# Kernel tuning notes

Hardware: AMD Instinct MI355X
Metric: run time of the kernel (lower is better)

The kernel has to match this reference:

```python
import jax, jax.numpy as jnp
import numpy as np

HIDDEN = 4096
N_HEADS = 32
N_KV_HEADS = 8
HEAD_DIM = 128
MAX_POS = 4096
N_GROUPS = N_HEADS // N_KV_HEADS  # 4


def _sincos_table():
    # create_sinusoidal_positions(MAX_POS, HEAD_DIM) -> [MAX_POS, 1, 2*HEAD_DIM]
    inv_freq = 1.0 / 10000 ** (np.arange(0, HEAD_DIM, 2) / HEAD_DIM)
    freqs = np.einsum('i,j->ij', np.arange(MAX_POS), inv_freq).astype('float32')
    emb = np.concatenate((freqs, freqs), axis=-1)  # [MAX_POS, HEAD_DIM]
    out = np.concatenate((np.sin(emb)[:, None, :], np.cos(emb)[:, None, :]), axis=-1)
    return jnp.asarray(out[:, :, :MAX_POS])  # slice is a no-op since 2*HEAD_DIM < MAX_POS

_SINCOS = _sincos_table()


def _rotate_half(t):
    half = t.shape[-1] // 2
    return jnp.concatenate((-t[..., half:], t[..., :half]), axis=-1)


def setup_inputs() -> dict:
    key = jax.random.key(0)
    ks = jax.random.split(key, 9)
    B, S = 1, 2048
    scale = 0.02
    return {
        'hidden_states': jax.random.normal(ks[0], (B, S, HIDDEN), jnp.float32),
        'attention_mask': jnp.ones((B, 1, 1, S), jnp.bool_),
        'position_ids': jnp.broadcast_to(jnp.arange(S, dtype=jnp.int32)[None, :], (B, S)),
        'Wq': jax.random.normal(ks[1], (HIDDEN, N_HEADS * HEAD_DIM), jnp.float32) * scale,
        'bq': jnp.zeros((N_HEADS * HEAD_DIM,), jnp.float32),
        'Wk': jax.random.normal(ks[2], (HIDDEN, N_KV_HEADS * HEAD_DIM), jnp.float32) * scale,
        'bk': jnp.zeros((N_KV_HEADS * HEAD_DIM,), jnp.float32),
        'Wv': jax.random.normal(ks[3], (HIDDEN, N_KV_HEADS * HEAD_DIM), jnp.float32) * scale,
        'bv': jnp.zeros((N_KV_HEADS * HEAD_DIM,), jnp.float32),
        'Wo': jax.random.normal(ks[4], (N_HEADS * HEAD_DIM, HIDDEN), jnp.float32) * scale,
        'bo': jnp.zeros((HIDDEN,), jnp.float32),
    }


def reference(hidden_states, attention_mask, position_ids, Wq, bq, Wk, bk, Wv, bv, Wo, bo):
    B, S, _ = hidden_states.shape
    # QKV projections + split heads
    q = (hidden_states @ Wq + bq).reshape(B, S, N_HEADS, HEAD_DIM)
    k = (hidden_states @ Wk + bk).reshape(B, S, N_KV_HEADS, HEAD_DIM)
    v = (hidden_states @ Wv + bv).reshape(B, S, N_KV_HEADS, HEAD_DIM)
    # Rotary embedding: sincos[position_ids] -> [B,S,1,2*HEAD_DIM]
    sincos = _SINCOS[position_ids]
    sin_pos, cos_pos = jnp.split(sincos, 2, axis=-1)  # each [B,S,1,HEAD_DIM]
    k = k * cos_pos + _rotate_half(k) * sin_pos
    q = q * cos_pos + _rotate_half(q) * sin_pos
    # Causal mask combined with padding mask
    causal = jnp.tril(jnp.ones((S, S), jnp.bool_))[None, None]  # [1,1,S,S]
    mask = jnp.logical_and(attention_mask, causal)  # [B,1,S,S]
    # GQA: repeat kv heads
    k = jnp.repeat(k, N_GROUPS, axis=2)  # [B,S,H,D]
    v = jnp.repeat(v, N_GROUPS, axis=2)
    bias = jnp.where(mask, 0.0, jnp.finfo(jnp.float32).min).astype(jnp.float32)
    scores = jnp.einsum('bqhd,bkhd->bhqk', q, k) / jnp.sqrt(jnp.float32(HEAD_DIM)) + bias
    attn_weights = jax.nn.softmax(scores, axis=-1)  # [B,H,S,S]
    attn_output = jnp.einsum('bhqk,bkhd->bqhd', attn_weights, v).reshape(B, S, N_HEADS * HEAD_DIM)
    return attn_output @ Wo + bo
```

## Files before the change

kernel.cpp:

```cpp
#include <hip/hip_runtime.h>
#include <hip/hip_bf16.h>
#include <math.h>

typedef __bf16 bf16x8 __attribute__((ext_vector_type(8)));
typedef __bf16 bf16x4 __attribute__((ext_vector_type(4)));
typedef float  f32x4  __attribute__((ext_vector_type(4)));
typedef unsigned int u32;

#define S_LEN 2048
#define HID   4096
#define NH    32
#define NKV   8
#define HD    128

__device__ inline void gld_lds16(const __bf16* g, __bf16* l) {
  __builtin_amdgcn_global_load_lds((const __attribute__((address_space(1))) u32*)g,
                                   (__attribute__((address_space(3))) u32*)l,
                                   16, 0, 0);
}

__global__ void cast_bf16(const float* __restrict__ in, __bf16* __restrict__ out, int n4) {
  int i = blockIdx.x * blockDim.x + threadIdx.x;
  if (i < n4) {
    float4 v = ((const float4*)in)[i];
    bf16x4 o;
    o[0] = (__bf16)v.x; o[1] = (__bf16)v.y; o[2] = (__bf16)v.z; o[3] = (__bf16)v.w;
    ((bf16x4*)out)[i] = o;
  }
}

template <typename T>
__global__ void transpose_cast(const T* __restrict__ in, __bf16* __restrict__ out,
                               int ldi, int ldo) {
  __shared__ float tile[32][33];
  const int c0 = blockIdx.x * 32, r0 = blockIdx.y * 32;
  const int tx = threadIdx.x, ty = threadIdx.y;
  for (int j = 0; j < 32; j += 8)
    tile[ty + j][tx] = (float)in[(size_t)(r0 + ty + j) * ldi + c0 + tx];
  __syncthreads();
  for (int j = 0; j < 32; j += 8)
    out[(size_t)(c0 + ty + j) * ldo + r0 + tx] = (__bf16)tile[tx][ty + j];
}

__global__ void concat_bias(const float* __restrict__ bk, const float* __restrict__ bv,
                            float* __restrict__ out) {
  int i = blockIdx.x * blockDim.x + threadIdx.x;
  if (i < 2048) out[i] = (i < 1024) ? bk[i] : bv[i - 1024];
}

template <typename CT>
__global__ __launch_bounds__(256) void gemm_bt(const __bf16* __restrict__ A,
                                               const __bf16* __restrict__ Bt,
                                               const float* __restrict__ bias,
                                               CT* __restrict__ C,
                                               int M, int N, int K) {
  __shared__ __bf16 As[128 * 32];
  __shared__ __bf16 Bs[128 * 32];
  const int tid  = threadIdx.x;
  const int lane = tid & 63;
  const int lrow = lane & 15, quad = lane >> 4;
  const int wave = tid >> 6;
  const int wm = (wave & 1) * 64, wn = (wave >> 1) * 64;
  const int m0 = blockIdx.y * 128, n0 = blockIdx.x * 128;

  f32x4 acc[4][4] = {};

  const int c1 = tid, c2 = tid + 256;
  const __bf16* a1 = A + (size_t)(m0 + (c1 >> 2)) * K + (c1 & 3) * 8;
  const __bf16* a2 = A + (size_t)(m0 + (c2 >> 2)) * K + (c2 & 3) * 8;
  const __bf16* b1 = Bt + (size_t)(n0 + (c1 >> 2)) * K + (c1 & 3) * 8;
  const __bf16* b2 = Bt + (size_t)(n0 + (c2 >> 2)) * K + (c2 & 3) * 8;
  __bf16* As1 = As + c1 * 8; __bf16* As2 = As + c2 * 8;
  __bf16* Bs1 = Bs + c1 * 8; __bf16* Bs2 = Bs + c2 * 8;

  for (int k0 = 0; k0 < K; k0 += 32) {
    __syncthreads();
    gld_lds16(a1 + k0, As1);
    gld_lds16(a2 + k0, As2);
    gld_lds16(b1 + k0, Bs1);
    gld_lds16(b2 + k0, Bs2);
    __syncthreads();

    bf16x8 af[4], bfr[4];
#pragma unroll
    for (int t = 0; t < 4; t++) {
      af[t]  = *(const bf16x8*)(As + (wm + t * 16 + lrow) * 32 + quad * 8);
      bfr[t] = *(const bf16x8*)(Bs + (wn + t * 16 + lrow) * 32 + quad * 8);
    }
#pragma unroll
    for (int i = 0; i < 4; i++)
#pragma unroll
      for (int j = 0; j < 4; j++)
        acc[i][j] = __builtin_amdgcn_mfma_f32_16x16x32_bf16(af[i], bfr[j], acc[i][j], 0, 0, 0);
  }

#pragma unroll
  for (int i = 0; i < 4; i++) {
    const int row = m0 + wm + i * 16 + quad * 4;
#pragma unroll
    for (int j = 0; j < 4; j++) {
      const int col = n0 + wn + j * 16 + lrow;
      const float b = bias[col];
#pragma unroll
      for (int r = 0; r < 4; r++)
        C[(size_t)(row + r) * N + col] = (CT)(acc[i][j][r] + b);
    }
  }
}

__global__ void rope_inplace(__bf16* __restrict__ Q, __bf16* __restrict__ KV,
                             const int* __restrict__ pos_ids) {
  const int s = blockIdx.y;
  const int t = blockIdx.x * blockDim.x + threadIdx.x;
  const int h = t >> 6, j = t & 63;
  const float pos = (float)pos_ids[s];
  const float inv_freq = __builtin_exp2f((float)j * -0.2076205059304601f);
  const float ang = pos * inv_freq;
  float sn, cs;
  sincosf(ang, &sn, &cs);
  if (h < NH) {
    __bf16* p = Q + (size_t)s * HID + h * HD + j;
    const float x0 = (float)p[0], x1 = (float)p[64];
    p[0]  = (__bf16)(x0 * cs - x1 * sn);
    p[64] = (__bf16)(x1 * cs + x0 * sn);
  } else {
    const int hk = h - NH;
    __bf16* p = KV + (size_t)s * 2048 + hk * HD + j;
    const float x0 = (float)p[0], x1 = (float)p[64];
    p[0]  = (__bf16)(x0 * cs - x1 * sn);
    p[64] = (__bf16)(x1 * cs + x0 * sn);
  }
}

__global__ __launch_bounds__(256) void flash_attn(const __bf16* __restrict__ Qb,
                                                  const __bf16* __restrict__ Kb,
                                                  const __bf16* __restrict__ Vt,
                                                  __bf16* __restrict__ attn, int ldk) {
  __shared__ __bf16 Ks[2][32 * 128];
  __shared__ __bf16 Vs[2][128 * 32];
  __shared__ __bf16 Plds[4][2][16][40];
  const int tid  = threadIdx.x;
  const int wave = tid >> 6;
  const int lane = tid & 63;
  const int lrow = lane & 15, quad = lane >> 4;

  const int c = blockIdx.x & 255, p = blockIdx.x >> 8;
  const int h = c >> 3;
  const int xh = c & 7;
  const int xx = p ? xh : 15 - xh;
  const int bq0 = xx * 128;
  const int kvh = h >> 2;
  const int T0 = bq0 + wave * 16;
  const int T1 = T0 + 64;
  const int kend = bq0 + 128;

  const int cK1 = tid, cK2 = tid + 256;
  const int cV1 = tid, cV2 = tid + 256;
  const __bf16* kg1 = Kb + (size_t)(cK1 & 31) * ldk + kvh * HD + (cK1 >> 5) * 8;
  const __bf16* kg2 = Kb + (size_t)(cK2 & 31) * ldk + kvh * HD + (cK2 >> 5) * 8;
  const __bf16* vg1 = Vt + (size_t)(kvh * HD + (cV1 & 127)) * S_LEN + (cV1 >> 7) * 8;
  const __bf16* vg2 = Vt + (size_t)(kvh * HD + (cV2 & 127)) * S_LEN + (cV2 >> 7) * 8;

  bf16x8 qf[2][4];
#pragma unroll
  for (int m = 0; m < 2; m++) {
    const __bf16* qbase = Qb + (size_t)(T0 + m * 64 + lrow) * HID + h * HD + quad * 8;
#pragma unroll
    for (int kc = 0; kc < 4; kc++) qf[m][kc] = *(const bf16x8*)(qbase + kc * 32);
  }

  f32x4 o[2][8] = {};
  f32x4 lac[2] = {};
  bf16x8 ones;
#pragma unroll
  for (int j = 0; j < 8; j++) ones[j] = (__bf16)1.0f;

  const float cs = 0.08838834764831845f * 1.44269504088896f;

  gld_lds16(kg1, &Ks[0][cK1 * 8]);
  gld_lds16(kg2, &Ks[0][cK2 * 8]);
  gld_lds16(vg1, &Vs[0][cV1 * 8]);
  gld_lds16(vg2, &Vs[0][cV2 * 8]);

  int cur = 0;
  for (int kb = 0; kb < kend; kb += 32) {
    __syncthreads();
    if (kb + 32 < kend) {
      const int nxt = cur ^ 1;
      gld_lds16(kg1 + (size_t)(kb + 32) * ldk, &Ks[nxt][cK1 * 8]);
      gld_lds16(kg2 + (size_t)(kb + 32) * ldk, &Ks[nxt][cK2 * 8]);
      gld_lds16(vg1 + (kb + 32), &Vs[nxt][cV1 * 8]);
      gld_lds16(vg2 + (kb + 32), &Vs[nxt][cV2 * 8]);
    }

    bf16x8 kf0[4], kf1[4];
#pragma unroll
    for (int kc = 0; kc < 4; kc++) {
      kf0[kc] = *(const bf16x8*)(&Ks[cur][((kc * 4 + quad) * 32 + lrow) * 8]);
      kf1[kc] = *(const bf16x8*)(&Ks[cur][((kc * 4 + quad) * 32 + 16 + lrow) * 8]);
    }
    f32x4 s[2][2] = {};
#pragma unroll
    for (int kc = 0; kc < 4; kc++) {
      s[0][0] = __builtin_amdgcn_mfma_f32_16x16x32_bf16(qf[0][kc], kf0[kc], s[0][0], 0, 0, 0);
      s[0][1] = __builtin_amdgcn_mfma_f32_16x16x32_bf16(qf[0][kc], kf1[kc], s[0][1], 0, 0, 0);
      s[1][0] = __builtin_amdgcn_mfma_f32_16x16x32_bf16(qf[1][kc], kf0[kc], s[1][0], 0, 0, 0);
      s[1][1] = __builtin_amdgcn_mfma_f32_16x16x32_bf16(qf[1][kc], kf1[kc], s[1][1], 0, 0, 0);
    }
#pragma unroll
    for (int m = 0; m < 2; m++) {
      const int Tm = m ? T1 : T0;
#pragma unroll
      for (int n = 0; n < 2; n++) {
        const int col = kb + n * 16 + lrow;
#pragma unroll
        for (int r = 0; r < 4; r++) {
          const int row = Tm + quad * 4 + r;
          const float pv = (col <= row) ? __builtin_exp2f(s[m][n][r] * cs) : 0.0f;
          Plds[wave][m][quad * 4 + r][n * 16 + lrow] = (__bf16)pv;
        }
      }
    }
    bf16x8 pf0 = *(const bf16x8*)(&Plds[wave][0][lrow][quad * 8]);
    bf16x8 pf1 = *(const bf16x8*)(&Plds[wave][1][lrow][quad * 8]);
#pragma unroll
    for (int dt = 0; dt < 8; dt++) {
      bf16x8 vf = *(const bf16x8*)(&Vs[cur][(quad * 128 + dt * 16 + lrow) * 8]);
      o[0][dt] = __builtin_amdgcn_mfma_f32_16x16x32_bf16(pf0, vf, o[0][dt], 0, 0, 0);
      o[1][dt] = __builtin_amdgcn_mfma_f32_16x16x32_bf16(pf1, vf, o[1][dt], 0, 0, 0);
    }
    lac[0] = __builtin_amdgcn_mfma_f32_16x16x32_bf16(pf0, ones, lac[0], 0, 0, 0);
    lac[1] = __builtin_amdgcn_mfma_f32_16x16x32_bf16(pf1, ones, lac[1], 0, 0, 0);
    cur ^= 1;
  }

#pragma unroll
  for (int m = 0; m < 2; m++) {
    const int Tm = m ? T1 : T0;
#pragma unroll
    for (int r = 0; r < 4; r++) {
      const float inv_l = 1.0f / lac[m][r];
      const size_t rowoff = (size_t)(Tm + quad * 4 + r) * HID + h * HD;
#pragma unroll
      for (int dt = 0; dt < 8; dt++)
        attn[rowoff + dt * 16 + lrow] = (__bf16)(o[m][dt][r] * inv_l);
    }
  }
}

extern "C" void kernel_launch(void* const* d_in, const int* in_sizes, int n_in,
                              void* d_out, int out_size, void* d_ws, size_t ws_size,
                              hipStream_t stream) {
  const float* hs = (const float*)d_in[0];
  const int* pos = (const int*)d_in[2];
  const float* Wq = (const float*)d_in[3];
  const float* bq = (const float*)d_in[4];
  const float* Wk = (const float*)d_in[5];
  const float* bk = (const float*)d_in[6];
  const float* Wv = (const float*)d_in[7];
  const float* bv = (const float*)d_in[8];
  const float* Wo = (const float*)d_in[9];
  const float* bo = (const float*)d_in[10];
  float* out = (float*)d_out;
  char* ws = (char*)d_ws;
  char* oc = (char*)d_out;

  __bf16* bHS   = (__bf16*)(ws + 0);
  __bf16* bWT   = (__bf16*)(ws + ((size_t)16 << 20));
  __bf16* bAttn = bHS;
  __bf16* bQ   = (__bf16*)(oc + 0);
  __bf16* bKV  = (__bf16*)(oc + ((size_t)16 << 20));
  __bf16* bVt  = (__bf16*)(oc + ((size_t)24 << 20));
  float*  bKVb = (float*)(oc + ((size_t)28 << 20));

  dim3 tb(32, 8);

  cast_bf16<<<8192, 256, 0, stream>>>(hs, bHS, (S_LEN * HID) / 4);
  transpose_cast<float><<<dim3(128, 128), tb, 0, stream>>>(Wq, bWT, 4096, 4096);
  gemm_bt<__bf16><<<dim3(32, 16), 256, 0, stream>>>(bHS, bWT, bq, bQ, 2048, 4096, 4096);
  transpose_cast<float><<<dim3(32, 128), tb, 0, stream>>>(Wk, bWT, 1024, 4096);
  transpose_cast<float><<<dim3(32, 128), tb, 0, stream>>>(Wv, bWT + (size_t)1024 * 4096, 1024, 4096);
  concat_bias<<<8, 256, 0, stream>>>(bk, bv, bKVb);
  gemm_bt<__bf16><<<dim3(16, 16), 256, 0, stream>>>(bHS, bWT, bKVb, bKV, 2048, 2048, 4096);
  rope_inplace<<<dim3(10, 2048), 256, 0, stream>>>(bQ, bKV, pos);
  transpose_cast<__bf16><<<dim3(32, 64), tb, 0, stream>>>(bKV + 1024, bVt, 2048, 2048);
  flash_attn<<<512, 256, 0, stream>>>(bQ, bKV, bVt, bAttn, 2048);
  transpose_cast<float><<<dim3(128, 128), tb, 0, stream>>>(Wo, bWT, 4096, 4096);
  gemm_bt<float><<<dim3(32, 16), 256, 0, stream>>>(bAttn, bWT, bo, out, 2048, 4096, 4096);
}
```

Before: 637.4 us.

## Deepen GEMM K tile and use rotated LDS layouts for GEMM and attention loads

The GEMM now stages a 64-wide K slice per iteration with four 16-byte loads per thread. The LDS tiles are row-major with a per-row rotation of the 8-element chunks, which is meant to avoid bank conflicts on MFMA fragment reads. The attention kernel switches its K and V LDS staging to the same rotated row-major scheme, with fragment offsets precomputed once per thread. This halves the number of barrier pairs in the GEMM and coalesces global reads, at the cost of doubled GEMM LDS and extra offset registers.

```diff
diff --git a/kernel.cpp b/kernel.cpp
--- a/kernel.cpp
+++ b/kernel.cpp
@@ -54,8 +54,8 @@
                                                const float* __restrict__ bias,
                                                CT* __restrict__ C,
                                                int M, int N, int K) {
-  __shared__ __bf16 As[128 * 32];
-  __shared__ __bf16 Bs[128 * 32];
+  __shared__ __bf16 As[128 * 64];
+  __shared__ __bf16 Bs[128 * 64];
   const int tid  = threadIdx.x;
   const int lane = tid & 63;
   const int lrow = lane & 15, quad = lane >> 4;
@@ -65,33 +65,55 @@
 
   f32x4 acc[4][4] = {};
 
-  const int c1 = tid, c2 = tid + 256;
-  const __bf16* a1 = A + (size_t)(m0 + (c1 >> 2)) * K + (c1 & 3) * 8;
-  const __bf16* a2 = A + (size_t)(m0 + (c2 >> 2)) * K + (c2 & 3) * 8;
-  const __bf16* b1 = Bt + (size_t)(n0 + (c1 >> 2)) * K + (c1 & 3) * 8;
-  const __bf16* b2 = Bt + (size_t)(n0 + (c2 >> 2)) * K + (c2 & 3) * 8;
-  __bf16* As1 = As + c1 * 8; __bf16* As2 = As + c2 * 8;
-  __bf16* Bs1 = Bs + c1 * 8; __bf16* Bs2 = Bs + c2 * 8;
-
-  for (int k0 = 0; k0 < K; k0 += 32) {
+  const __bf16* aP[4];
+  const __bf16* bP[4];
+  __bf16* aL[4];
+  __bf16* bL[4];
+#pragma unroll
+  for (int s = 0; s < 4; s++) {
+    const int c = tid + 256 * s;
+    const int row = c >> 3;
+    const int kc = ((c & 7) + row) & 7;
+    aP[s] = A + (size_t)(m0 + row) * K + kc * 8;
+    bP[s] = Bt + (size_t)(n0 + row) * K + kc * 8;
+    aL[s] = As + c * 8;
+    bL[s] = Bs + c * 8;
+  }
+
+  int offA[2][4], offB[2][4];
+#pragma unroll
+  for (int h = 0; h < 2; h++)
+#pragma unroll
+    for (int t = 0; t < 4; t++) {
+      const int ra = wm + t * 16 + lrow;
+      const int rb = wn + t * 16 + lrow;
+      offA[h][t] = (ra * 8 + ((h * 4 + quad - ra) & 7)) * 8;
+      offB[h][t] = (rb * 8 + ((h * 4 + quad - rb) & 7)) * 8;
+    }
+
+  for (int k0 = 0; k0 < K; k0 += 64) {
     __syncthreads();
-    gld_lds16(a1 + k0, As1);
-    gld_lds16(a2 + k0, As2);
-    gld_lds16(b1 + k0, Bs1);
-    gld_lds16(b2 + k0, Bs2);
+#pragma unroll
+    for (int s = 0; s < 4; s++) {
+      gld_lds16(aP[s] + k0, aL[s]);
+      gld_lds16(bP[s] + k0, bL[s]);
+    }
     __syncthreads();
 
-    bf16x8 af[4], bfr[4];
-#pragma unroll
-    for (int t = 0; t < 4; t++) {
-      af[t]  = *(const bf16x8*)(As + (wm + t * 16 + lrow) * 32 + quad * 8);
-      bfr[t] = *(const bf16x8*)(Bs + (wn + t * 16 + lrow) * 32 + quad * 8);
-    }
-#pragma unroll
-    for (int i = 0; i < 4; i++)
-#pragma unroll
-      for (int j = 0; j < 4; j++)
-        acc[i][j] = __builtin_amdgcn_mfma_f32_16x16x32_bf16(af[i], bfr[j], acc[i][j], 0, 0, 0);
+#pragma unroll
+    for (int h = 0; h < 2; h++) {
+      bf16x8 af[4], bfr[4];
+#pragma unroll
+      for (int t = 0; t < 4; t++) {
+        af[t]  = *(const bf16x8*)(As + offA[h][t]);
+        bfr[t] = *(const bf16x8*)(Bs + offB[h][t]);
+      }
+#pragma unroll
+      for (int i = 0; i < 4; i++)
+#pragma unroll
+        for (int j = 0; j < 4; j++)
+          acc[i][j] = __builtin_amdgcn_mfma_f32_16x16x32_bf16(af[i], bfr[j], acc[i][j], 0, 0, 0);
+    }
   }
 
 #pragma unroll
@@ -154,12 +176,34 @@
   const int T1 = T0 + 64;
   const int kend = bq0 + 128;
 
-  const int cK1 = tid, cK2 = tid + 256;
-  const int cV1 = tid, cV2 = tid + 256;
-  const __bf16* kg1 = Kb + (size_t)(cK1 & 31) * ldk + kvh * HD + (cK1 >> 5) * 8;
-  const __bf16* kg2 = Kb + (size_t)(cK2 & 31) * ldk + kvh * HD + (cK2 >> 5) * 8;
-  const __bf16* vg1 = Vt + (size_t)(kvh * HD + (cV1 & 127)) * S_LEN + (cV1 >> 7) * 8;
-  const __bf16* vg2 = Vt + (size_t)(kvh * HD + (cV2 & 127)) * S_LEN + (cV2 >> 7) * 8;
+  const __bf16* kg[2];
+  const __bf16* vg[2];
+  __bf16* kL[2];
+  __bf16* vL[2];
+#pragma unroll
+  for (int s = 0; s < 2; s++) {
+    const int ck = tid + 256 * s;
+    const int key = ck >> 4, kcb = ((ck & 15) + key) & 15;
+    kg[s] = Kb + (size_t)key * ldk + kvh * HD + kcb * 8;
+    kL[s] = (__bf16*)0 + ck * 8;
+    const int cv = tid + 256 * s;
+    const int d = cv >> 2, vcb = ((cv & 3) + d) & 3;
+    vg[s] = Vt + (size_t)(kvh * HD + d) * S_LEN + vcb * 8;
+    vL[s] = (__bf16*)0 + cv * 8;
+  }
+
+  int offK0[4], offK1[4], offV[8];
+#pragma unroll
+  for (int kc = 0; kc < 4; kc++) {
+    const int rot = (kc * 4 + quad - lrow) & 15;
+    offK0[kc] = (lrow * 16 + rot) * 8;
+    offK1[kc] = ((lrow + 16) * 16 + rot) * 8;
+  }
+#pragma unroll
+  for (int dt = 0; dt < 8; dt++) {
+    const int d = dt * 16 + lrow;
+    offV[dt] = (d * 4 + ((quad - d) & 3)) * 8;
+  }
 
   bf16x8 qf[2][4];
 #pragma unroll
@@ -177,27 +221,29 @@
 
   const float cs = 0.08838834764831845f * 1.44269504088896f;
 
-  gld_lds16(kg1, &Ks[0][cK1 * 8]);
-  gld_lds16(kg2, &Ks[0][cK2 * 8]);
-  gld_lds16(vg1, &Vs[0][cV1 * 8]);
-  gld_lds16(vg2, &Vs[0][cV2 * 8]);
+#pragma unroll
+  for (int s = 0; s < 2; s++) {
+    gld_lds16(kg[s], &Ks[0][0] + (size_t)(kL[s] - (__bf16*)0));
+    gld_lds16(vg[s], &Vs[0][0] + (size_t)(vL[s] - (__bf16*)0));
+  }
 
   int cur = 0;
   for (int kb = 0; kb < kend; kb += 32) {
     __syncthreads();
     if (kb + 32 < kend) {
       const int nxt = cur ^ 1;
-      gld_lds16(kg1 + (size_t)(kb + 32) * ldk, &Ks[nxt][cK1 * 8]);
-      gld_lds16(kg2 + (size_t)(kb + 32) * ldk, &Ks[nxt][cK2 * 8]);
-      gld_lds16(vg1 + (kb + 32), &Vs[nxt][cV1 * 8]);
-      gld_lds16(vg2 + (kb + 32), &Vs[nxt][cV2 * 8]);
+#pragma unroll
+      for (int s = 0; s < 2; s++) {
+        gld_lds16(kg[s] + (size_t)(kb + 32) * ldk, &Ks[nxt][0] + (size_t)(kL[s] - (__bf16*)0));
+        gld_lds16(vg[s] + (kb + 32), &Vs[nxt][0] + (size_t)(vL[s] - (__bf16*)0));
+      }
     }
 
     bf16x8 kf0[4], kf1[4];
 #pragma unroll
     for (int kc = 0; kc < 4; kc++) {
-      kf0[kc] = *(const bf16x8*)(&Ks[cur][((kc * 4 + quad) * 32 + lrow) * 8]);
-      kf1[kc] = *(const bf16x8*)(&Ks[cur][((kc * 4 + quad) * 32 + 16 + lrow) * 8]);
+      kf0[kc] = *(const bf16x8*)(&Ks[cur][offK0[kc]]);
+      kf1[kc] = *(const bf16x8*)(&Ks[cur][offK1[kc]]);
     }
     f32x4 s[2][2] = {};
 #pragma unroll
@@ -225,7 +271,7 @@
     bf16x8 pf1 = *(const bf16x8*)(&Plds[wave][1][lrow][quad * 8]);
 #pragma unroll
     for (int dt = 0; dt < 8; dt++) {
-      bf16x8 vf = *(const bf16x8*)(&Vs[cur][(quad * 128 + dt * 16 + lrow) * 8]);
+      bf16x8 vf = *(const bf16x8*)(&Vs[cur][offV[dt]]);
       o[0][dt] = __builtin_amdgcn_mfma_f32_16x16x32_bf16(pf0, vf, o[0][dt], 0, 0, 0);
       o[1][dt] = __builtin_amdgcn_mfma_f32_16x16x32_bf16(pf1, vf, o[1][dt], 0, 0, 0);
     }
```

Result: faster. 567.6 us (-11.0%).
